# Kernel optimization log

Measured on AMD Instinct MI355X. Metric: run time of the kernel, lower is better.

The kernel has to match this reference:

```python
import jax, jax.numpy as jnp
import numpy as np

IN_FEATURES = 4096
OUT_FEATURES = 11008


def setup_inputs() -> dict:
    key = jax.random.key(0)
    kx, kw, ks, kb = jax.random.split(key, 4)
    x = jax.random.normal(kx, (64, IN_FEATURES), dtype=jnp.float32)
    # int8 quantized weight, stored as int32 for portability (values in [-128, 127])
    weight_quantized = jax.random.randint(kw, (OUT_FEATURES, IN_FEATURES), -128, 128, dtype=jnp.int32)
    # per-tensor scale, as produced by quantize_weights_int8: |w|.max()/127
    weight_scale = jnp.asarray(0.01, dtype=jnp.float32)
    bias = jax.random.normal(kb, (OUT_FEATURES,), dtype=jnp.float32) * 0.02
    return {"x": x, "weight_quantized": weight_quantized, "weight_scale": weight_scale, "bias": bias}


def reference(x, weight_quantized, weight_scale, bias):
    # dequantize_weights_int8: q.float() * scale, then F.linear(x, W, b) = x @ W.T + b
    weight = weight_quantized.astype(jnp.float32) * weight_scale  # [out, in]
    return jnp.einsum('mi,oi->mo', x, weight) + bias
```

## Files before the change

kernel.cpp:

```cpp
#include <hip/hip_runtime.h>
#include <hip/hip_bf16.h>


#define M_DIM 64
#define N_DIM 11008
#define K_DIM 4096
#define KC (K_DIM / 4)

typedef __attribute__((ext_vector_type(8))) short bf16x8;
typedef __attribute__((ext_vector_type(4))) float f32x4;
typedef __attribute__((ext_vector_type(4))) int i32x4;
typedef __attribute__((ext_vector_type(8))) short s16x8;

__device__ __forceinline__ short f2bf(float f) {
    unsigned int u = __builtin_bit_cast(unsigned int, f);
    u = u + 0x7FFFu + ((u >> 16) & 1u);
    return (short)(u >> 16);
}
__device__ __forceinline__ short i2bf(int q) {
    float f = (float)q;
    return (short)(__builtin_bit_cast(unsigned int, f) >> 16);
}

__global__ __launch_bounds__(256) void convert_x_kernel(const float* __restrict__ x,
                                                        short* __restrict__ xs) {
    int idx = blockIdx.x * 256 + threadIdx.x;
    const f32x4* p = (const f32x4*)x + (size_t)idx * 2;
    f32x4 a = p[0], b = p[1];
    s16x8 h;
    h[0] = f2bf(a.x); h[1] = f2bf(a.y); h[2] = f2bf(a.z); h[3] = f2bf(a.w);
    h[4] = f2bf(b.x); h[5] = f2bf(b.y); h[6] = f2bf(b.z); h[7] = f2bf(b.w);
    *((s16x8*)xs + idx) = h;
}

__global__ __launch_bounds__(256) void qgemm_kernel(const short* __restrict__ xs,
                                                    const int* __restrict__ wq,
                                                    const float* __restrict__ scale_p,
                                                    const float* __restrict__ bias,
                                                    float* __restrict__ out) {
    __shared__ float red[4][16][64];

    const int t    = threadIdx.x;
    const int wv   = t >> 6;
    const int lane = t & 63;
    const int quad = lane >> 4;
    const int l16  = lane & 15;
    const int n0   = blockIdx.x * 16;

    const int kbase = wv * KC;
    const int* wp = wq + (size_t)(n0 + l16) * K_DIM + kbase + quad * 8;
    const short* xp = xs + (size_t)l16 * K_DIM + kbase + quad * 8;

    f32x4 acc[4] = {f32x4{0,0,0,0}, f32x4{0,0,0,0}, f32x4{0,0,0,0}, f32x4{0,0,0,0}};

    i32x4 w0 = __builtin_nontemporal_load((const i32x4*)(wp));
    i32x4 w1 = __builtin_nontemporal_load((const i32x4*)(wp + 4));
    bf16x8 af[4];
    #pragma unroll
    for (int mi = 0; mi < 4; ++mi)
        af[mi] = *(const bf16x8*)(xp + (size_t)mi * 16 * K_DIM);

    for (int kk = 0; kk < KC; kk += 32) {
        const int nk = (kk + 32 < KC) ? (kk + 32) : kk;
        i32x4 nw0 = __builtin_nontemporal_load((const i32x4*)(wp + nk));
        i32x4 nw1 = __builtin_nontemporal_load((const i32x4*)(wp + nk + 4));
        bf16x8 naf[4];
        #pragma unroll
        for (int mi = 0; mi < 4; ++mi)
            naf[mi] = *(const bf16x8*)(xp + (size_t)mi * 16 * K_DIM + nk);

        bf16x8 bfrag;
        bfrag[0] = i2bf(w0.x); bfrag[1] = i2bf(w0.y);
        bfrag[2] = i2bf(w0.z); bfrag[3] = i2bf(w0.w);
        bfrag[4] = i2bf(w1.x); bfrag[5] = i2bf(w1.y);
        bfrag[6] = i2bf(w1.z); bfrag[7] = i2bf(w1.w);

        #pragma unroll
        for (int mi = 0; mi < 4; ++mi)
            acc[mi] = __builtin_amdgcn_mfma_f32_16x16x32_bf16(af[mi], bfrag, acc[mi], 0, 0, 0);

        w0 = nw0; w1 = nw1;
        #pragma unroll
        for (int mi = 0; mi < 4; ++mi) af[mi] = naf[mi];
    }

    #pragma unroll
    for (int mi = 0; mi < 4; ++mi)
        *(f32x4*)&red[wv][l16][mi * 16 + quad * 4] = acc[mi];
    __syncthreads();

    {
        const int n  = t & 15;
        const int mg = t >> 4;
        f32x4 s0 = *(const f32x4*)&red[0][n][mg * 4];
        f32x4 s1 = *(const f32x4*)&red[1][n][mg * 4];
        f32x4 s2 = *(const f32x4*)&red[2][n][mg * 4];
        f32x4 s3 = *(const f32x4*)&red[3][n][mg * 4];
        const float sc = *scale_p;
        const float b  = bias[n0 + n];
        #pragma unroll
        for (int j = 0; j < 4; ++j) {
            float v = (s0[j] + s1[j] + s2[j] + s3[j]) * sc + b;
            out[(size_t)(mg * 4 + j) * N_DIM + n0 + n] = v;
        }
    }
}

extern "C" void kernel_launch(void* const* d_in, const int* in_sizes, int n_in,
                              void* d_out, int out_size, void* d_ws, size_t ws_size,
                              hipStream_t stream) {
    const float* x     = (const float*)d_in[0];
    const int*   wq    = (const int*)d_in[1];
    const float* scale = (const float*)d_in[2];
    const float* bias  = (const float*)d_in[3];
    float* out = (float*)d_out;

    short* xs = (short*)d_ws;

    convert_x_kernel<<<128, 256, 0, stream>>>(x, xs);
    qgemm_kernel<<<N_DIM / 16, 256, 0, stream>>>(xs, wq, scale, bias, out);
}
```

Before: 290.7 us.

## Deepen weight/activation prefetch to four-stage ring and duplicate grid along y

Replaces the single-step register double buffer with a four-slot ring of prefetched weight and activation fragments, using an unrolled main loop and a drain tail. The aim is to keep more global loads in flight and hide memory latency. The weight loads also drop the nontemporal hint and become plain loads. The grid gains a second y dimension of 2, which makes every block pair compute and write identical outputs. That doubles weight and activation reads unless the caches absorb them, and it adds register pressure from the deeper buffers.

```diff
diff --git a/kernel.cpp b/kernel.cpp
--- a/kernel.cpp
+++ b/kernel.cpp
@@ -6,6 +6,8 @@
 #define N_DIM 11008
 #define K_DIM 4096
 #define KC (K_DIM / 4)
+#define PF 4
+#define DUP 2
 
 typedef __attribute__((ext_vector_type(8))) short bf16x8;
 typedef __attribute__((ext_vector_type(4))) float f32x4;
@@ -20,6 +22,12 @@
 __device__ __forceinline__ short i2bf(int q) {
     float f = (float)q;
     return (short)(__builtin_bit_cast(unsigned int, f) >> 16);
+}
+__device__ __forceinline__ bf16x8 cvt_w(i32x4 a, i32x4 b) {
+    bf16x8 r;
+    r[0] = i2bf(a.x); r[1] = i2bf(a.y); r[2] = i2bf(a.z); r[3] = i2bf(a.w);
+    r[4] = i2bf(b.x); r[5] = i2bf(b.y); r[6] = i2bf(b.z); r[7] = i2bf(b.w);
+    return r;
 }
 
 __global__ __launch_bounds__(256) void convert_x_kernel(const float* __restrict__ x,
@@ -53,35 +61,39 @@
 
     f32x4 acc[4] = {f32x4{0,0,0,0}, f32x4{0,0,0,0}, f32x4{0,0,0,0}, f32x4{0,0,0,0}};
 
-    i32x4 w0 = __builtin_nontemporal_load((const i32x4*)(wp));
-    i32x4 w1 = __builtin_nontemporal_load((const i32x4*)(wp + 4));
-    bf16x8 af[4];
+    i32x4  wb[PF][2];
+    bf16x8 ab[PF][4];
+
     #pragma unroll
-    for (int mi = 0; mi < 4; ++mi)
-        af[mi] = *(const bf16x8*)(xp + (size_t)mi * 16 * K_DIM);
-
-    for (int kk = 0; kk < KC; kk += 32) {
-        const int nk = (kk + 32 < KC) ? (kk + 32) : kk;
-        i32x4 nw0 = __builtin_nontemporal_load((const i32x4*)(wp + nk));
-        i32x4 nw1 = __builtin_nontemporal_load((const i32x4*)(wp + nk + 4));
-        bf16x8 naf[4];
+    for (int p = 0; p < PF; ++p) {
+        wb[p][0] = *(const i32x4*)(wp + p * 32);
+        wb[p][1] = *(const i32x4*)(wp + p * 32 + 4);
         #pragma unroll
         for (int mi = 0; mi < 4; ++mi)
-            naf[mi] = *(const bf16x8*)(xp + (size_t)mi * 16 * K_DIM + nk);
+            ab[p][mi] = *(const bf16x8*)(xp + (size_t)mi * 16 * K_DIM + p * 32);
+    }
 
-        bf16x8 bfrag;
-        bfrag[0] = i2bf(w0.x); bfrag[1] = i2bf(w0.y);
-        bfrag[2] = i2bf(w0.z); bfrag[3] = i2bf(w0.w);
-        bfrag[4] = i2bf(w1.x); bfrag[5] = i2bf(w1.y);
-        bfrag[6] = i2bf(w1.z); bfrag[7] = i2bf(w1.w);
-
+    #pragma unroll 4
+    for (int kk = 0; kk < KC - PF * 32; kk += 32) {
+        const int slot = (kk >> 5) & (PF - 1);
+        bf16x8 bfrag = cvt_w(wb[slot][0], wb[slot][1]);
         #pragma unroll
         for (int mi = 0; mi < 4; ++mi)
-            acc[mi] = __builtin_amdgcn_mfma_f32_16x16x32_bf16(af[mi], bfrag, acc[mi], 0, 0, 0);
-
-        w0 = nw0; w1 = nw1;
+            acc[mi] = __builtin_amdgcn_mfma_f32_16x16x32_bf16(ab[slot][mi], bfrag, acc[mi], 0, 0, 0);
+        const int kn = kk + PF * 32;
+        wb[slot][0] = *(const i32x4*)(wp + kn);
+        wb[slot][1] = *(const i32x4*)(wp + kn + 4);
         #pragma unroll
-        for (int mi = 0; mi < 4; ++mi) af[mi] = naf[mi];
+        for (int mi = 0; mi < 4; ++mi)
+            ab[slot][mi] = *(const bf16x8*)(xp + (size_t)mi * 16 * K_DIM + kn);
+    }
+    #pragma unroll
+    for (int p = 0; p < PF; ++p) {
+        const int slot = (KC / 32 - PF + p) & (PF - 1);
+        bf16x8 bfrag = cvt_w(wb[slot][0], wb[slot][1]);
+        #pragma unroll
+        for (int mi = 0; mi < 4; ++mi)
+            acc[mi] = __builtin_amdgcn_mfma_f32_16x16x32_bf16(ab[slot][mi], bfrag, acc[mi], 0, 0, 0);
     }
 
     #pragma unroll
@@ -118,5 +130,7 @@
     short* xs = (short*)d_ws;
 
     convert_x_kernel<<<128, 256, 0, stream>>>(x, xs);
-    qgemm_kernel<<<N_DIM / 16, 256, 0, stream>>>(xs, wq, scale, bias, out);
+
+    dim3 grid(N_DIM / 16, DUP);
+    qgemm_kernel<<<grid, 256, 0, stream>>>(xs, wq, scale, bias, out);
 }
```

New measurement: 335.2 us. +15.3%, slower.
